# Kernel optimization log

Hardware: AMD Instinct MI355X
Metric: run time of the kernel (lower is better)

Reference implementation:

```python
import jax, jax.numpy as jnp
import numpy as np

NUM_EXPERTS = 64
TOP_K = 2
AUX_LOSS_COEF = 0.01
Z_LOSS_COEF = 0.001


def setup_inputs() -> dict:
    key = jax.random.key(0)
    k1, k2 = jax.random.split(key)
    hidden_states = jax.random.normal(k1, (4, 4096, 4096), dtype=jnp.float32)
    # nn.Linear(hidden_size, num_experts, bias=False) -> weight [E, H]
    gate_w = jax.random.normal(k2, (NUM_EXPERTS, 4096), dtype=jnp.float32) * 0.02
    return {"hidden_states": hidden_states, "gate_w": gate_w}


def reference(hidden_states, gate_w):
    b, s, h = hidden_states.shape
    # gate projection: [b, s, E]
    router_logits = jnp.einsum("bsh,eh->bse", hidden_states, gate_w)
    # softmax in fp32 as in the torch module
    probs = jax.nn.softmax(router_logits.astype(jnp.float32), axis=-1)
    routing_weights, selected_experts = jax.lax.top_k(probs, TOP_K)
    routing_weights = routing_weights / jnp.sum(routing_weights, axis=-1, keepdims=True)
    routing_weights = routing_weights.astype(hidden_states.dtype)

    # auxiliary load-balancing loss
    num_tokens = b * s
    # scatter_(-1, selected, 1): top-k indices are distinct, so one_hot-sum == set-to-1
    expert_mask = jax.nn.one_hot(selected_experts, NUM_EXPERTS, dtype=router_logits.dtype).sum(axis=-2)  # [b,s,E]
    tokens_per_expert = expert_mask.sum(axis=(0, 1)) / num_tokens          # [E]
    router_prob_per_expert = probs.sum(axis=(0, 1)) / num_tokens           # [E]
    aux_loss = NUM_EXPERTS * jnp.sum(tokens_per_expert * router_prob_per_expert)

    # z-loss: mean of squared logsumexp over experts
    z_loss = jnp.mean(jax.scipy.special.logsumexp(router_logits, axis=-1) ** 2)

    router_loss = AUX_LOSS_COEF * aux_loss + Z_LOSS_COEF * z_loss
    return routing_weights, selected_experts, router_loss
```

## Files before the change

kernel.cpp:

```cpp
#include <hip/hip_runtime.h>
#include <math.h>

#define HDIM 4096
#define NEXP 64
#define NTOK 16384
#define MBLK 64
#define KC   64
#define NCHUNK (HDIM / KC)
#define CSTRIDE 68

typedef float v4f __attribute__((ext_vector_type(4)));
typedef short bh4 __attribute__((ext_vector_type(4)));
typedef float f32x16 __attribute__((ext_vector_type(16)));

#if defined(__has_builtin)
#if __has_builtin(__builtin_amdgcn_mfma_f32_32x32x8bf16_1k)
#define HAVE_MFMA_BUILTIN 1
#endif
#endif

__device__ __forceinline__ f32x16 mfma_bf16(bh4 a, bh4 b, f32x16 c) {
#ifdef HAVE_MFMA_BUILTIN
    return __builtin_amdgcn_mfma_f32_32x32x8bf16_1k(a, b, c, 0, 0, 0);
#else
    asm("v_mfma_f32_32x32x8_bf16 %0, %1, %2, %0" : "+v"(c) : "v"(a), "v"(b));
    return c;
#endif
}

__device__ __forceinline__ void barrier_lgkm_only() {
    asm volatile("s_waitcnt lgkmcnt(0)\n\ts_barrier" ::: "memory");
}

__device__ __forceinline__ void split3(float v, unsigned short& h0,
                                       unsigned short& h1, unsigned short& h2) {
    unsigned b0 = __builtin_bit_cast(unsigned, v);
    unsigned r0 = (b0 + 0x7FFFu + ((b0 >> 16) & 1u)) & 0xFFFF0000u;
    h0 = (unsigned short)(r0 >> 16);
    float v1 = v - __builtin_bit_cast(float, r0);
    unsigned b1 = __builtin_bit_cast(unsigned, v1);
    unsigned r1 = (b1 + 0x7FFFu + ((b1 >> 16) & 1u)) & 0xFFFF0000u;
    h1 = (unsigned short)(r1 >> 16);
    float v2 = v1 - __builtin_bit_cast(float, r1);
    h2 = (unsigned short)(__builtin_bit_cast(unsigned, v2) >> 16);
}

__global__ __launch_bounds__(512, 1) void router_main(
    const float* __restrict__ hidden,
    const float* __restrict__ gate,
    float* __restrict__ out_rw,
    float* __restrict__ out_sel,
    float* __restrict__ psum_g,
    float* __restrict__ cnt_g,
    float* __restrict__ zsum_g)
{
    __shared__ uint2 frag[2][2][3][2][8][64];
    __shared__ float Pacc[4][16][64];
    __shared__ float C_lds[MBLK * CSTRIDE];
    __shared__ float rden[MBLK];
    __shared__ unsigned hist[NEXP];

    const int t = threadIdx.x;
    const int lane = t & 63;
    const int wave = __builtin_amdgcn_readfirstlane(t >> 6);
    const int m0 = blockIdx.x * MBLK;
    const int c = wave & 3, h = wave >> 2;
    const int mtp = c & 1, ntp = c >> 1;

    const v4f* __restrict__ A4 = (const v4f*)hidden;
    const v4f* __restrict__ G4 = (const v4f*)gate;

    const int sr = t >> 3;
    const int sk = t & 7;
    const size_t abase = (size_t)(m0 + sr) * (HDIM / 4) + sk * 2;
    const size_t gbase = (size_t)sr * (HDIM / 4) + sk * 2;

    auto stage = [&](int buf, int ab, v4f x0, v4f x1) {
        float av[8] = {x0.x, x0.y, x0.z, x0.w, x1.x, x1.y, x1.z, x1.w};
        unsigned short hs[3][8];
#pragma unroll
        for (int u = 0; u < 8; ++u) split3(av[u], hs[0][u], hs[1][u], hs[2][u]);
        const int half = sr >> 5, rl = sr & 31;
#pragma unroll
        for (int p = 0; p < 3; ++p) {
            frag[buf][ab][p][half][sk][rl ^ (sk << 3)] =
                make_uint2((unsigned)hs[p][0] | ((unsigned)hs[p][1] << 16),
                           (unsigned)hs[p][2] | ((unsigned)hs[p][3] << 16));
            frag[buf][ab][p][half][sk][(32 + rl) ^ (sk << 3)] =
                make_uint2((unsigned)hs[p][4] | ((unsigned)hs[p][5] << 16),
                           (unsigned)hs[p][6] | ((unsigned)hs[p][7] << 16));
        }
    };

    v4f pa0 = __builtin_nontemporal_load(&A4[abase]);
    v4f pa1 = __builtin_nontemporal_load(&A4[abase + 1]);
    v4f pg0 = G4[gbase];
    v4f pg1 = G4[gbase + 1];
    stage(0, 0, pa0, pa1);
    stage(0, 1, pg0, pg1);
    pa0 = __builtin_nontemporal_load(&A4[abase + 16]);
    pa1 = __builtin_nontemporal_load(&A4[abase + 17]);
    pg0 = G4[gbase + 16];
    pg1 = G4[gbase + 17];
    __syncthreads();

    f32x16 acc{};

    for (int it = 0; it < NCHUNK; ++it) {
        const int cur = it & 1;
        if (it + 1 < NCHUNK) {
            stage(cur ^ 1, 0, pa0, pa1);
            stage(cur ^ 1, 1, pg0, pg1);
        }
        if (it + 2 < NCHUNK) {
            const size_t off = (size_t)(it + 2) * 16;
            pa0 = __builtin_nontemporal_load(&A4[abase + off]);
            pa1 = __builtin_nontemporal_load(&A4[abase + off + 1]);
            pg0 = G4[gbase + off];
            pg1 = G4[gbase + off + 1];
        }
#pragma unroll
        for (int s = 0; s < 4; ++s) {
            const int k8 = h * 4 + s;
            const int slot = lane ^ (k8 << 3);
            bh4 a0 = __builtin_bit_cast(bh4, frag[cur][0][0][mtp][k8][slot]);
            bh4 a1 = __builtin_bit_cast(bh4, frag[cur][0][1][mtp][k8][slot]);
            bh4 a2 = __builtin_bit_cast(bh4, frag[cur][0][2][mtp][k8][slot]);
            bh4 b0 = __builtin_bit_cast(bh4, frag[cur][1][0][ntp][k8][slot]);
            bh4 b1 = __builtin_bit_cast(bh4, frag[cur][1][1][ntp][k8][slot]);
            bh4 b2 = __builtin_bit_cast(bh4, frag[cur][1][2][ntp][k8][slot]);
            acc = mfma_bf16(a0, b0, acc);
            acc = mfma_bf16(a1, b0, acc);
            acc = mfma_bf16(a0, b1, acc);
            acc = mfma_bf16(a1, b1, acc);
            acc = mfma_bf16(a2, b0, acc);
            acc = mfma_bf16(a0, b2, acc);
        }
        barrier_lgkm_only();
    }

    asm volatile("s_nop 7\n\ts_nop 7\n\ts_nop 7" :::);

    if (h == 1) {
#pragma unroll
        for (int r = 0; r < 16; ++r) Pacc[c][r][lane] = acc[r];
    }
    if (t < NEXP) hist[t] = 0u;
    __syncthreads();
    if (h == 0) {
#pragma unroll
        for (int r = 0; r < 16; ++r) {
            float x = acc[r] + Pacc[c][r][lane];
            const int tok = mtp * 32 + (r & 3) + 8 * (r >> 2) + 4 * (lane >> 5);
            const int e = ntp * 32 + (lane & 31);
            C_lds[tok * CSTRIDE + e] = x;
        }
    }
    __syncthreads();

    if (wave != 0) return;

    float z = 0.f;
    {
        float v1 = -INFINITY, v2 = -INFINITY;
        int i1 = 0, i2 = 0;
        for (int e = 0; e < NEXP; ++e) {
            float v = C_lds[lane * CSTRIDE + e];
            if (v > v1)      { v2 = v1; i2 = i1; v1 = v; i1 = e; }
            else if (v > v2) { v2 = v;  i2 = e; }
        }
        atomicAdd(&hist[i1], 1u);
        atomicAdd(&hist[i2], 1u);

        float d = 0.f;
        for (int e = 0; e < NEXP; ++e) {
            float ev = expf(C_lds[lane * CSTRIDE + e] - v1);
            C_lds[lane * CSTRIDE + e] = ev;
            d += ev;
        }
        rden[lane] = 1.0f / d;
        float lse = v1 + logf(d);
        z = lse * lse;

        float e2 = expf(v2 - v1);
        float w2 = e2 / (1.f + e2);
        float w1 = 1.f - w2;
        int tok = m0 + lane;
        out_rw[2 * tok + 0] = w1;
        out_rw[2 * tok + 1] = w2;
        out_sel[2 * tok + 0] = (float)i1;
        out_sel[2 * tok + 1] = (float)i2;
    }

#pragma unroll
    for (int off = 32; off > 0; off >>= 1) z += __shfl_down(z, off);
    if (lane == 0) atomicAdd(zsum_g, z);

    float ps = 0.f;
    for (int m = 0; m < MBLK; ++m)
        ps += C_lds[m * CSTRIDE + lane] * rden[m];
    atomicAdd(&psum_g[lane], ps);
    atomicAdd(&cnt_g[lane], (float)hist[lane]);
}

__global__ void router_final(const float* __restrict__ ws, float* __restrict__ out_loss)
{
    int e = threadIdx.x;
    const float inv = 1.0f / (float)NTOK;
    float p = (ws[64 + e] * inv) * (ws[e] * inv);
#pragma unroll
    for (int off = 32; off > 0; off >>= 1) p += __shfl_down(p, off);
    if (e == 0)
        out_loss[0] = 0.01f * (64.f * p) + 0.001f * (ws[128] * inv);
}

extern "C" void kernel_launch(void* const* d_in, const int* in_sizes, int n_in,
                              void* d_out, int out_size, void* d_ws, size_t ws_size,
                              hipStream_t stream) {
    const float* hidden = (const float*)d_in[0];
    const float* gate   = (const float*)d_in[1];
    float* out = (float*)d_out;
    float* ws  = (float*)d_ws;

    hipMemsetAsync(d_ws, 0, 129 * sizeof(float), stream);
    router_main<<<dim3(NTOK / MBLK), dim3(512), 0, stream>>>(
        hidden, gate,
        out,
        out + NTOK * 2,
        ws, ws + 64, ws + 128);
    router_final<<<dim3(1), dim3(64), 0, stream>>>(ws, out + NTOK * 4);
}
```

Baseline: 429.9 us.

## Pre-split gate weights once, use 2-term bf16 split, shrink blocks for occupancy

Adds a small kernel that splits the gate matrix into hi/lo bf16 MFMA fragments in workspace once per call. The main kernel then loads B fragments straight from global memory into registers instead of re-splitting the gate in every block. The fp32 emulation drops from a 3-term to a 2-term split, cutting MFMAs from 6 to 4 per k-step. Blocks shrink to 32 tokens and 256 threads with up to 4 blocks per CU, trading per-block reuse for occupancy. The 2-term split lowers logit accuracy, which could flip top-k choices on near-tied experts.

```diff
diff --git a/kernel.cpp b/kernel.cpp
--- a/kernel.cpp
+++ b/kernel.cpp
@@ -4,10 +4,10 @@
 #define HDIM 4096
 #define NEXP 64
 #define NTOK 16384
-#define MBLK 64
-#define KC   64
-#define NCHUNK (HDIM / KC)
+#define MBLK 32
+#define NCHUNK 64
 #define CSTRIDE 68
+#define GS_FLOATS 262144
 
 typedef float v4f __attribute__((ext_vector_type(4)));
 typedef short bh4 __attribute__((ext_vector_type(4)));
@@ -32,30 +32,50 @@
     asm volatile("s_waitcnt lgkmcnt(0)\n\ts_barrier" ::: "memory");
 }
 
-__device__ __forceinline__ void split3(float v, unsigned short& h0,
-                                       unsigned short& h1, unsigned short& h2) {
+__device__ __forceinline__ void split2(float v, unsigned short& h0,
+                                       unsigned short& h1) {
     unsigned b0 = __builtin_bit_cast(unsigned, v);
     unsigned r0 = (b0 + 0x7FFFu + ((b0 >> 16) & 1u)) & 0xFFFF0000u;
     h0 = (unsigned short)(r0 >> 16);
     float v1 = v - __builtin_bit_cast(float, r0);
     unsigned b1 = __builtin_bit_cast(unsigned, v1);
-    unsigned r1 = (b1 + 0x7FFFu + ((b1 >> 16) & 1u)) & 0xFFFF0000u;
-    h1 = (unsigned short)(r1 >> 16);
-    float v2 = v1 - __builtin_bit_cast(float, r1);
-    h2 = (unsigned short)(__builtin_bit_cast(unsigned, v2) >> 16);
-}
-
-__global__ __launch_bounds__(512, 1) void router_main(
+    h1 = (unsigned short)((b1 + 0x7FFFu + ((b1 >> 16) & 1u)) >> 16);
+}
+
+__device__ __forceinline__ uint2 pack4(const unsigned short* h) {
+    return make_uint2((unsigned)h[0] | ((unsigned)h[1] << 16),
+                      (unsigned)h[2] | ((unsigned)h[3] << 16));
+}
+
+__global__ __launch_bounds__(256) void gate_presplit(
+    const float* __restrict__ gate, uint2* __restrict__ gs)
+{
+    const int f = blockIdx.x * 256 + threadIdx.x;
+    const int l = f & 63;
+    const int ntp = (f >> 6) & 1;
+    const int k8g = f >> 7;
+    const int e = ntp * 32 + (l & 31);
+    const int k = k8g * 8 + (l >> 5) * 4;
+    v4f x = *(const v4f*)&gate[(size_t)e * HDIM + k];
+    float xv[4] = {x.x, x.y, x.z, x.w};
+    unsigned short lo[4], hi[4];
+#pragma unroll
+    for (int j = 0; j < 4; ++j) split2(xv[j], lo[j], hi[j]);
+    gs[((size_t)(k8g * 2 + 0) * 2 + ntp) * 64 + l] = pack4(lo);
+    gs[((size_t)(k8g * 2 + 1) * 2 + ntp) * 64 + l] = pack4(hi);
+}
+
+__global__ __launch_bounds__(256, 4) void router_main(
     const float* __restrict__ hidden,
-    const float* __restrict__ gate,
+    const uint2* __restrict__ gs,
     float* __restrict__ out_rw,
     float* __restrict__ out_sel,
     float* __restrict__ psum_g,
     float* __restrict__ cnt_g,
     float* __restrict__ zsum_g)
 {
-    __shared__ uint2 frag[2][2][3][2][8][64];
-    __shared__ float Pacc[4][16][64];
+    __shared__ uint2 Af[2][8][2][64];
+    __shared__ float Pacc[2][16][64];
     __shared__ float C_lds[MBLK * CSTRIDE];
     __shared__ float rden[MBLK];
     __shared__ unsigned hist[NEXP];
@@ -63,95 +83,92 @@
     const int t = threadIdx.x;
     const int lane = t & 63;
     const int wave = __builtin_amdgcn_readfirstlane(t >> 6);
+    const int ntp = wave & 1, h = wave >> 1;
     const int m0 = blockIdx.x * MBLK;
-    const int c = wave & 3, h = wave >> 2;
-    const int mtp = c & 1, ntp = c >> 1;
 
     const v4f* __restrict__ A4 = (const v4f*)hidden;
-    const v4f* __restrict__ G4 = (const v4f*)gate;
-
-    const int sr = t >> 3;
-    const int sk = t & 7;
-    const size_t abase = (size_t)(m0 + sr) * (HDIM / 4) + sk * 2;
-    const size_t gbase = (size_t)sr * (HDIM / 4) + sk * 2;
-
-    auto stage = [&](int buf, int ab, v4f x0, v4f x1) {
+
+    const int row = t >> 3;
+    const int k8s = t & 7;
+    const size_t abase = (size_t)(m0 + row) * (HDIM / 4) + k8s * 2;
+    const int sw_w = (k8s & 1) << 3;
+
+    auto stageA = [&](int buf, v4f x0, v4f x1) {
         float av[8] = {x0.x, x0.y, x0.z, x0.w, x1.x, x1.y, x1.z, x1.w};
-        unsigned short hs[3][8];
-#pragma unroll
-        for (int u = 0; u < 8; ++u) split3(av[u], hs[0][u], hs[1][u], hs[2][u]);
-        const int half = sr >> 5, rl = sr & 31;
-#pragma unroll
-        for (int p = 0; p < 3; ++p) {
-            frag[buf][ab][p][half][sk][rl ^ (sk << 3)] =
-                make_uint2((unsigned)hs[p][0] | ((unsigned)hs[p][1] << 16),
-                           (unsigned)hs[p][2] | ((unsigned)hs[p][3] << 16));
-            frag[buf][ab][p][half][sk][(32 + rl) ^ (sk << 3)] =
-                make_uint2((unsigned)hs[p][4] | ((unsigned)hs[p][5] << 16),
-                           (unsigned)hs[p][6] | ((unsigned)hs[p][7] << 16));
-        }
+        unsigned short lo[8], hi[8];
+#pragma unroll
+        for (int u = 0; u < 8; ++u) split2(av[u], lo[u], hi[u]);
+        const int s0 = row ^ sw_w;
+        Af[buf][k8s][0][s0]      = pack4(lo);
+        Af[buf][k8s][0][s0 + 32] = pack4(lo + 4);
+        Af[buf][k8s][1][s0]      = pack4(hi);
+        Af[buf][k8s][1][s0 + 32] = pack4(hi + 4);
     };
 
-    v4f pa0 = __builtin_nontemporal_load(&A4[abase]);
-    v4f pa1 = __builtin_nontemporal_load(&A4[abase + 1]);
-    v4f pg0 = G4[gbase];
-    v4f pg1 = G4[gbase + 1];
-    stage(0, 0, pa0, pa1);
-    stage(0, 1, pg0, pg1);
-    pa0 = __builtin_nontemporal_load(&A4[abase + 16]);
-    pa1 = __builtin_nontemporal_load(&A4[abase + 17]);
-    pg0 = G4[gbase + 16];
-    pg1 = G4[gbase + 17];
+    f32x16 acc{};
+
+    v4f ap0 = __builtin_nontemporal_load(&A4[abase]);
+    v4f ap1 = __builtin_nontemporal_load(&A4[abase + 1]);
+    stageA(0, ap0, ap1);
+    ap0 = __builtin_nontemporal_load(&A4[abase + 16]);
+    ap1 = __builtin_nontemporal_load(&A4[abase + 17]);
+
+    uint2 bA[8], bB[8];
+#pragma unroll
+    for (int s = 0; s < 4; ++s) {
+        const int k8g = h * 4 + s;
+        bA[2 * s + 0] = gs[((size_t)(k8g * 2 + 0) * 2 + ntp) * 64 + lane];
+        bA[2 * s + 1] = gs[((size_t)(k8g * 2 + 1) * 2 + ntp) * 64 + lane];
+    }
     __syncthreads();
 
-    f32x16 acc{};
-
-    for (int it = 0; it < NCHUNK; ++it) {
+    auto step = [&](int it, uint2 (&bc)[8], uint2 (&bn)[8]) {
         const int cur = it & 1;
-        if (it + 1 < NCHUNK) {
-            stage(cur ^ 1, 0, pa0, pa1);
-            stage(cur ^ 1, 1, pg0, pg1);
-        }
-        if (it + 2 < NCHUNK) {
-            const size_t off = (size_t)(it + 2) * 16;
-            pa0 = __builtin_nontemporal_load(&A4[abase + off]);
-            pa1 = __builtin_nontemporal_load(&A4[abase + off + 1]);
-            pg0 = G4[gbase + off];
-            pg1 = G4[gbase + off + 1];
-        }
+        const int cn = (it + 1 < NCHUNK) ? it + 1 : NCHUNK - 1;
+#pragma unroll
+        for (int s = 0; s < 4; ++s) {
+            const int k8g = cn * 8 + h * 4 + s;
+            bn[2 * s + 0] = gs[((size_t)(k8g * 2 + 0) * 2 + ntp) * 64 + lane];
+            bn[2 * s + 1] = gs[((size_t)(k8g * 2 + 1) * 2 + ntp) * 64 + lane];
+        }
+        if (it + 1 < NCHUNK) stageA(cur ^ 1, ap0, ap1);
+        const int ca = (it + 2 < NCHUNK) ? it + 2 : NCHUNK - 1;
+        ap0 = __builtin_nontemporal_load(&A4[abase + (size_t)ca * 16]);
+        ap1 = __builtin_nontemporal_load(&A4[abase + (size_t)ca * 16 + 1]);
 #pragma unroll
         for (int s = 0; s < 4; ++s) {
             const int k8 = h * 4 + s;
-            const int slot = lane ^ (k8 << 3);
-            bh4 a0 = __builtin_bit_cast(bh4, frag[cur][0][0][mtp][k8][slot]);
-            bh4 a1 = __builtin_bit_cast(bh4, frag[cur][0][1][mtp][k8][slot]);
-            bh4 a2 = __builtin_bit_cast(bh4, frag[cur][0][2][mtp][k8][slot]);
-            bh4 b0 = __builtin_bit_cast(bh4, frag[cur][1][0][ntp][k8][slot]);
-            bh4 b1 = __builtin_bit_cast(bh4, frag[cur][1][1][ntp][k8][slot]);
-            bh4 b2 = __builtin_bit_cast(bh4, frag[cur][1][2][ntp][k8][slot]);
+            const int slot = lane ^ ((k8 & 1) << 3);
+            bh4 a0 = __builtin_bit_cast(bh4, Af[cur][k8][0][slot]);
+            bh4 a1 = __builtin_bit_cast(bh4, Af[cur][k8][1][slot]);
+            bh4 b0 = __builtin_bit_cast(bh4, bc[2 * s + 0]);
+            bh4 b1 = __builtin_bit_cast(bh4, bc[2 * s + 1]);
             acc = mfma_bf16(a0, b0, acc);
             acc = mfma_bf16(a1, b0, acc);
             acc = mfma_bf16(a0, b1, acc);
             acc = mfma_bf16(a1, b1, acc);
-            acc = mfma_bf16(a2, b0, acc);
-            acc = mfma_bf16(a0, b2, acc);
         }
         barrier_lgkm_only();
-    }
-
-    asm volatile("s_nop 7\n\ts_nop 7\n\ts_nop 7" :::);
+    };
+
+    for (int it = 0; it < NCHUNK; it += 2) {
+        step(it, bA, bB);
+        step(it + 1, bB, bA);
+    }
+
+    asm volatile("s_nop 7\n\ts_nop 7" :::);
 
     if (h == 1) {
 #pragma unroll
-        for (int r = 0; r < 16; ++r) Pacc[c][r][lane] = acc[r];
+        for (int r = 0; r < 16; ++r) Pacc[ntp][r][lane] = acc[r];
     }
     if (t < NEXP) hist[t] = 0u;
     __syncthreads();
     if (h == 0) {
 #pragma unroll
         for (int r = 0; r < 16; ++r) {
-            float x = acc[r] + Pacc[c][r][lane];
-            const int tok = mtp * 32 + (r & 3) + 8 * (r >> 2) + 4 * (lane >> 5);
+            float x = acc[r] + Pacc[ntp][r][lane];
+            const int tok = (r & 3) + 8 * (r >> 2) + 4 * (lane >> 5);
             const int e = ntp * 32 + (lane & 31);
             C_lds[tok * CSTRIDE + e] = x;
         }
@@ -161,7 +178,7 @@
     if (wave != 0) return;
 
     float z = 0.f;
-    {
+    if (lane < MBLK) {
         float v1 = -INFINITY, v2 = -INFINITY;
         int i1 = 0, i2 = 0;
         for (int e = 0; e < NEXP; ++e) {
@@ -221,12 +238,14 @@
     const float* gate   = (const float*)d_in[1];
     float* out = (float*)d_out;
     float* ws  = (float*)d_ws;
-
-    hipMemsetAsync(d_ws, 0, 129 * sizeof(float), stream);
-    router_main<<<dim3(NTOK / MBLK), dim3(512), 0, stream>>>(
-        hidden, gate,
+    float* stats = ws + GS_FLOATS;
+
+    hipMemsetAsync(stats, 0, 129 * sizeof(float), stream);
+    gate_presplit<<<dim3(256), dim3(256), 0, stream>>>(gate, (uint2*)ws);
+    router_main<<<dim3(NTOK / MBLK), dim3(256), 0, stream>>>(
+        hidden, (const uint2*)ws,
         out,
         out + NTOK * 2,
-        ws, ws + 64, ws + 128);
-    router_final<<<dim3(1), dim3(64), 0, stream>>>(ws, out + NTOK * 4);
-}
+        stats, stats + 64, stats + 128);
+    router_final<<<dim3(1), dim3(64), 0, stream>>>(stats, out + NTOK * 4);
+}
```

New measurement: 402.2 us. 1.07x faster.
